# Kernel tuning notes

Hardware: AMD Instinct MI355X
Metric: run time of the kernel (lower is better)

The kernel has to match this reference:

```python
import jax, jax.numpy as jnp
import numpy as np

B, S, D, H = 2, 2048, 768, 12
E = D // H  # d_head = 64


def setup_inputs() -> dict:
    key = jax.random.key(0)
    ks = jax.random.split(key, 10)
    scale = 1.0 / np.sqrt(D)
    x = jax.random.normal(ks[0], (B, S, D), dtype=jnp.float32)
    # Additive mask, laid out [H*B, S, S] as the torch forward slices per head.
    attn_mask = jnp.zeros((H * B, S, S), dtype=jnp.float32)
    # Per-head projections (math form: q = x @ Wq[h] + bq[h])
    Wq = jax.random.normal(ks[1], (H, D, E), dtype=jnp.float32) * scale
    bq = jax.random.normal(ks[2], (H, E), dtype=jnp.float32) * 0.01
    Wk = jax.random.normal(ks[3], (H, D, E), dtype=jnp.float32) * scale
    bk = jax.random.normal(ks[4], (H, E), dtype=jnp.float32) * 0.01
    Wv = jax.random.normal(ks[5], (H, D, E), dtype=jnp.float32) * scale
    bv = jax.random.normal(ks[6], (H, E), dtype=jnp.float32) * 0.01
    Wo = jax.random.normal(ks[7], (D, D), dtype=jnp.float32) * scale
    bo = jax.random.normal(ks[8], (D,), dtype=jnp.float32) * 0.01
    return {"x": x, "attn_mask": attn_mask, "Wq": Wq, "bq": bq,
            "Wk": Wk, "bk": bk, "Wv": Wv, "bv": bv, "Wo": Wo, "bo": bo}


def reference(x, attn_mask, Wq, bq, Wk, bk, Wv, bv, Wo, bo):
    # x: [B,S,D]; attn_mask: [H*B,S,S]
    q = jnp.einsum('bsd,hde->hbse', x, Wq) + bq[:, None, None, :]
    k = jnp.einsum('bsd,hde->hbse', x, Wk) + bk[:, None, None, :]
    v = jnp.einsum('bsd,hde->hbse', x, Wv) + bv[:, None, None, :]
    mask = attn_mask.reshape(H, B, S, S)
    # NOTE: original code has NO 1/sqrt(d_head) scaling — kept faithful.
    logits = jnp.einsum('hbse,hbte->hbst', q, k) + mask
    w = jax.nn.softmax(logits, axis=-1)  # dropout is identity at eval / p=0
    o = jnp.einsum('hbst,hbte->hbse', w, v)  # [H,B,S,E]
    o = jnp.transpose(o, (1, 2, 0, 3)).reshape(B, S, H * E)  # concat heads
    return o @ Wo + bo
```

## Files before the change

kernel.cpp:

```cpp
#include <hip/hip_runtime.h>
#include <hip/hip_bf16.h>
#include <cmath>

constexpr int Bc  = 2;
constexpr int Sc  = 2048;
constexpr int Dc  = 768;
constexpr int Hc  = 12;
constexpr int Ec  = 64;
constexpr int BSc = Bc * Sc;

typedef _Float16 f16;
typedef __attribute__((ext_vector_type(8)))  _Float16 half8;
typedef __attribute__((ext_vector_type(16))) float    floatx16;

__global__ __launch_bounds__(256) void prep_kernel(
    const float* __restrict__ x,
    const float* __restrict__ Wq, const float* __restrict__ Wk, const float* __restrict__ Wv,
    const float* __restrict__ bq, const float* __restrict__ bk, const float* __restrict__ bv,
    const float* __restrict__ Wo,
    f16* __restrict__ x16, f16* __restrict__ Wt16, f16* __restrict__ Wot16,
    float* __restrict__ bias_cat)
{
    __shared__ __align__(16) float Ts[64][65];
    const int t = threadIdx.x;
    int bid = blockIdx.x;

    if (bid < 1536) {
        const size_t base = (size_t)bid * 2048 + t * 8;
        const float4 v0 = *(const float4*)(x + base);
        const float4 v1 = *(const float4*)(x + base + 4);
        half8 hv;
        hv[0] = (f16)v0.x; hv[1] = (f16)v0.y; hv[2] = (f16)v0.z; hv[3] = (f16)v0.w;
        hv[4] = (f16)v1.x; hv[5] = (f16)v1.y; hv[6] = (f16)v1.z; hv[7] = (f16)v1.w;
        *(half8*)(x16 + base) = hv;
        return;
    }
    bid -= 1536;
    if (bid < 432) {
        const int proj = bid / 144, rem = bid % 144, h = rem / 12, dt = rem % 12;
        const float* W = ((proj == 0) ? Wq : (proj == 1) ? Wk : Wv) + (size_t)h * Dc * Ec;
        const int c = t & 63, rr = t >> 6;
        #pragma unroll
        for (int r0 = 0; r0 < 64; r0 += 4) {
            const int d = rr + r0;
            Ts[d][c] = W[(size_t)(dt * 64 + d) * Ec + c];
        }
        __syncthreads();
        #pragma unroll
        for (int r0 = 0; r0 < 64; r0 += 4) {
            const int e = rr + r0;
            Wt16[(size_t)(proj * 768 + h * 64 + e) * Dc + dt * 64 + c] = (f16)Ts[c][e];
        }
        return;
    }
    bid -= 432;
    if (bid < 144) {
        const int rt = bid / 12, ct = bid % 12;
        const int c = t & 63, rr = t >> 6;
        #pragma unroll
        for (int r0 = 0; r0 < 64; r0 += 4) {
            const int d = rr + r0;
            Ts[d][c] = Wo[(size_t)(rt * 64 + d) * Dc + ct * 64 + c];
        }
        __syncthreads();
        #pragma unroll
        for (int r0 = 0; r0 < 64; r0 += 4) {
            const int e = rr + r0;
            Wot16[(size_t)(ct * 64 + e) * Dc + rt * 64 + c] = (f16)Ts[c][e];
        }
        return;
    }
    bid -= 144;
    {
        const int g = bid * 256 + t;
        if (g < 3 * 768) {
            const int proj = g / 768, idx = g % 768;
            const float* bb = (proj == 0) ? bq : (proj == 1) ? bk : bv;
            bias_cat[g] = bb[idx];
        }
    }
}

__global__ __launch_bounds__(256, 2) void gemm_qkv_kernel(
    const f16* __restrict__ x16, const f16* __restrict__ Wt16,
    const float* __restrict__ bias_cat,
    f16* __restrict__ q16, f16* __restrict__ k16, f16* __restrict__ v16t)
{
    __shared__ __align__(16) unsigned char smem[36864];
    f16 (*As)[72]  = (f16(*)[72])smem;
    f16 (*Bs)[72]  = (f16(*)[72])(smem + 18432);
    f16 (*Cs)[136] = (f16(*)[136])smem;

    const int t = threadIdx.x;
    const int wave = t >> 6, lane = t & 63;
    const int col = lane & 31, hf = lane >> 5;
    const int wr = wave & 1, wc = wave >> 1;
    const int m0 = blockIdx.x * 128, n0 = blockIdx.y * 128;

    floatx16 c00, c01, c10, c11;
    #pragma unroll
    for (int i = 0; i < 16; ++i) { c00[i] = 0.f; c01[i] = 0.f; c10[i] = 0.f; c11[i] = 0.f; }

    for (int k0 = 0; k0 < Dc; k0 += 64) {
        #pragma unroll
        for (int p = 0; p < 4; ++p) {
            const int cid = p * 256 + t;
            const int row = cid >> 3, seg = cid & 7;
            *(half8*)&As[row][seg * 8] =
                *(const half8*)(x16 + (size_t)(m0 + row) * Dc + k0 + seg * 8);
            *(half8*)&Bs[row][seg * 8] =
                *(const half8*)(Wt16 + (size_t)(n0 + row) * Dc + k0 + seg * 8);
        }
        __syncthreads();
        #pragma unroll
        for (int ks = 0; ks < 4; ++ks) {
            const half8 a0 = *(const half8*)&As[wr * 64 + col][ks * 16 + hf * 8];
            const half8 a1 = *(const half8*)&As[wr * 64 + 32 + col][ks * 16 + hf * 8];
            const half8 b0 = *(const half8*)&Bs[wc * 64 + col][ks * 16 + hf * 8];
            const half8 b1 = *(const half8*)&Bs[wc * 64 + 32 + col][ks * 16 + hf * 8];
            c00 = __builtin_amdgcn_mfma_f32_32x32x16_f16(a0, b0, c00, 0, 0, 0);
            c01 = __builtin_amdgcn_mfma_f32_32x32x16_f16(a0, b1, c01, 0, 0, 0);
            c10 = __builtin_amdgcn_mfma_f32_32x32x16_f16(a1, b0, c10, 0, 0, 0);
            c11 = __builtin_amdgcn_mfma_f32_32x32x16_f16(a1, b1, c11, 0, 0, 0);
        }
        __syncthreads();
    }

    const float bias0 = bias_cat[n0 + wc * 64 + col];
    const float bias1 = bias_cat[n0 + wc * 64 + 32 + col];
    #pragma unroll
    for (int i = 0; i < 16; ++i) {
        const int r = (i & 3) + 8 * (i >> 2) + 4 * hf;
        Cs[wr * 64 + r][wc * 64 + col]           = (f16)(c00[i] + bias0);
        Cs[wr * 64 + r][wc * 64 + 32 + col]      = (f16)(c01[i] + bias1);
        Cs[wr * 64 + 32 + r][wc * 64 + col]      = (f16)(c10[i] + bias0);
        Cs[wr * 64 + 32 + r][wc * 64 + 32 + col] = (f16)(c11[i] + bias1);
    }
    __syncthreads();

    const int proj = n0 / 768;
    const int h0   = (n0 - proj * 768) >> 6;
    const int b    = m0 >> 11;
    const int s_in = m0 & 2047;

    if (proj < 2) {
        f16* dst = (proj == 0) ? q16 : k16;
        const int row = t >> 1, seg = t & 1;
        const int h = h0 + seg;
        f16* gp = dst + ((size_t)(h * Bc + b) * Sc + s_in + row) * Ec;
        #pragma unroll
        for (int j = 0; j < 8; ++j)
            *(half8*)(gp + j * 8) = *(const half8*)&Cs[row][seg * 64 + j * 8];
    } else {
        const int coln = t & 127, half_ = t >> 7;
        const int seg = coln >> 6, e = coln & 63;
        const int h = h0 + seg;
        f16* gp = v16t + ((size_t)(h * Bc + b) * Ec + e) * Sc + s_in + half_ * 64;
        #pragma unroll
        for (int jb = 0; jb < 8; ++jb) {
            half8 tv;
            #pragma unroll
            for (int j2 = 0; j2 < 8; ++j2)
                tv[j2] = Cs[half_ * 64 + jb * 8 + j2][coln];
            *(half8*)(gp + jb * 8) = tv;
        }
    }
}

__global__ __launch_bounds__(256, 2) void flash_attn_kernel(
    const f16* __restrict__ q16, const f16* __restrict__ k16,
    const f16* __restrict__ v16t, const float* __restrict__ mask,
    f16* __restrict__ obuf16)
{
    __shared__ _Float16 Plds[4][32][40];
    __shared__ float MLds[2][64][17];
    __shared__ float LLds[2][64][17];
    __shared__ float OLds[2][64][33];

    const int rb   = blockIdx.x;
    const int b    = blockIdx.y;
    const int h    = blockIdx.z;
    const int hb   = h * Bc + b;
    const int t    = threadIdx.x;
    const int wave = t >> 6;
    const int lane = t & 63;
    const int rg   = wave & 1;
    const int kh   = wave >> 1;
    const int col  = lane & 31;
    const int hf   = lane >> 5;
    const int row0 = rb * 64 + rg * 32;

    const f16* qb = q16 + ((size_t)hb * Sc + row0) * Ec;
    const f16* kb = k16 + (size_t)hb * Sc * Ec;
    const f16* vb = v16t + (size_t)hb * Ec * Sc;

    half8 qfrag[4];
    #pragma unroll
    for (int ks = 0; ks < 4; ++ks)
        qfrag[ks] = *(const half8*)(qb + (size_t)col * Ec + ks * 16 + hf * 8);

    floatx16 o0, o1;
    float mrun[16], lrun[16];
    #pragma unroll
    for (int i = 0; i < 16; ++i) { o0[i] = 0.f; o1[i] = 0.f; mrun[i] = -1e30f; lrun[i] = 0.f; }

    const float* mbase = mask + ((size_t)hb * Sc + row0) * Sc + col;
    const int key_base = kh * (Sc / 2);
    constexpr int NT = (Sc / 2) / 32;

    float mbuf[16];
    #pragma unroll
    for (int i = 0; i < 16; ++i) {
        const int r = (i & 3) + 8 * (i >> 2) + 4 * hf;
        mbuf[i] = mbase[(size_t)r * Sc + key_base];
    }

    for (int kt = 0; kt < NT; ++kt) {
        const int key0 = key_base + kt * 32;

        float mcur[16];
        #pragma unroll
        for (int i = 0; i < 16; ++i) mcur[i] = mbuf[i];
        if (kt + 1 < NT) {
            #pragma unroll
            for (int i = 0; i < 16; ++i) {
                const int r = (i & 3) + 8 * (i >> 2) + 4 * hf;
                mbuf[i] = mbase[(size_t)r * Sc + key0 + 32];
            }
        }

        floatx16 c;
        #pragma unroll
        for (int i = 0; i < 16; ++i) c[i] = 0.f;
        #pragma unroll
        for (int ks = 0; ks < 4; ++ks) {
            const half8 kf = *(const half8*)(kb + (size_t)(key0 + col) * Ec + ks * 16 + hf * 8);
            c = __builtin_amdgcn_mfma_f32_32x32x16_f16(qfrag[ks], kf, c, 0, 0, 0);
        }

        float p[16];
        #pragma unroll
        for (int i = 0; i < 16; ++i) {
            const float s = c[i] + mcur[i];
            float v = s;
            v = fmaxf(v, __shfl_xor(v, 1));
            v = fmaxf(v, __shfl_xor(v, 2));
            v = fmaxf(v, __shfl_xor(v, 4));
            v = fmaxf(v, __shfl_xor(v, 8));
            v = fmaxf(v, __shfl_xor(v, 16));
            const float mnew  = fmaxf(mrun[i], v);
            const float alpha = __expf(mrun[i] - mnew);
            const float pe    = __expf(s - mnew);
            mrun[i] = mnew;
            float su = pe;
            su += __shfl_xor(su, 1);
            su += __shfl_xor(su, 2);
            su += __shfl_xor(su, 4);
            su += __shfl_xor(su, 8);
            su += __shfl_xor(su, 16);
            lrun[i] = lrun[i] * alpha + su;
            o0[i] *= alpha;
            o1[i] *= alpha;
            p[i] = pe;
        }

        #pragma unroll
        for (int i = 0; i < 16; ++i) {
            const int r = (i & 3) + 8 * (i >> 2) + 4 * hf;
            Plds[wave][r][col] = (f16)p[i];
        }
        asm volatile("s_waitcnt lgkmcnt(0)" ::: "memory");

        #pragma unroll
        for (int ks = 0; ks < 2; ++ks) {
            const half8 pf = *(const half8*)(&Plds[wave][col][ks * 16 + hf * 8]);
            const half8 v0 = *(const half8*)(vb + (size_t)col        * Sc + key0 + ks * 16 + hf * 8);
            const half8 v1 = *(const half8*)(vb + (size_t)(32 + col) * Sc + key0 + ks * 16 + hf * 8);
            o0 = __builtin_amdgcn_mfma_f32_32x32x16_f16(pf, v0, o0, 0, 0, 0);
            o1 = __builtin_amdgcn_mfma_f32_32x32x16_f16(pf, v1, o1, 0, 0, 0);
        }
    }

    if (kh == 1) {
        #pragma unroll
        for (int i = 0; i < 16; ++i) {
            MLds[rg][lane][i]      = mrun[i];
            LLds[rg][lane][i]      = lrun[i];
            OLds[rg][lane][i]      = o0[i];
            OLds[rg][lane][16 + i] = o1[i];
        }
    }
    __syncthreads();
    if (kh == 0) {
        #pragma unroll
        for (int i = 0; i < 16; ++i) {
            const float m2 = MLds[rg][lane][i];
            const float l2 = LLds[rg][lane][i];
            const float mn = fmaxf(mrun[i], m2);
            const float a1 = __expf(mrun[i] - mn);
            const float a2 = __expf(m2 - mn);
            const float inv = 1.f / (lrun[i] * a1 + l2 * a2);
            const float r0 = (o0[i] * a1 + OLds[rg][lane][i]      * a2) * inv;
            const float r1 = (o1[i] * a1 + OLds[rg][lane][16 + i] * a2) * inv;
            const int r = (i & 3) + 8 * (i >> 2) + 4 * hf;
            const size_t orow = ((size_t)b * Sc + row0 + r) * Dc + h * Ec;
            obuf16[orow + col]      = (f16)r0;
            obuf16[orow + 32 + col] = (f16)r1;
        }
    }
}

__global__ __launch_bounds__(256, 2) void gemm_out_kernel(
    const f16* __restrict__ a16, const f16* __restrict__ Wot16,
    const float* __restrict__ bo, float* __restrict__ out)
{
    __shared__ __align__(16) f16 As[128][72];
    __shared__ __align__(16) f16 Bs[64][72];

    const int t = threadIdx.x;
    const int wave = t >> 6, lane = t & 63;
    const int col = lane & 31, hf = lane >> 5;
    const int m0 = blockIdx.x * 128, n0 = blockIdx.y * 64;

    floatx16 c0, c1;
    #pragma unroll
    for (int i = 0; i < 16; ++i) { c0[i] = 0.f; c1[i] = 0.f; }

    for (int k0 = 0; k0 < Dc; k0 += 64) {
        #pragma unroll
        for (int p = 0; p < 4; ++p) {
            const int cid = p * 256 + t;
            *(half8*)&As[cid >> 3][(cid & 7) * 8] =
                *(const half8*)(a16 + (size_t)(m0 + (cid >> 3)) * Dc + k0 + (cid & 7) * 8);
        }
        #pragma unroll
        for (int p = 0; p < 2; ++p) {
            const int cid = p * 256 + t;
            *(half8*)&Bs[cid >> 3][(cid & 7) * 8] =
                *(const half8*)(Wot16 + (size_t)(n0 + (cid >> 3)) * Dc + k0 + (cid & 7) * 8);
        }
        __syncthreads();
        #pragma unroll
        for (int ks = 0; ks < 4; ++ks) {
            const half8 a  = *(const half8*)&As[wave * 32 + col][ks * 16 + hf * 8];
            const half8 b0 = *(const half8*)&Bs[col][ks * 16 + hf * 8];
            const half8 b1 = *(const half8*)&Bs[32 + col][ks * 16 + hf * 8];
            c0 = __builtin_amdgcn_mfma_f32_32x32x16_f16(a, b0, c0, 0, 0, 0);
            c1 = __builtin_amdgcn_mfma_f32_32x32x16_f16(a, b1, c1, 0, 0, 0);
        }
        __syncthreads();
    }

    const float bo0 = bo[n0 + col], bo1 = bo[n0 + 32 + col];
    #pragma unroll
    for (int i = 0; i < 16; ++i) {
        const int r = (i & 3) + 8 * (i >> 2) + 4 * hf;
        const size_t ro = (size_t)(m0 + wave * 32 + r) * Dc + n0;
        out[ro + col]      = c0[i] + bo0;
        out[ro + 32 + col] = c1[i] + bo1;
    }
}

extern "C" void kernel_launch(void* const* d_in, const int* in_sizes, int n_in,
                              void* d_out, int out_size, void* d_ws, size_t ws_size,
                              hipStream_t stream)
{
    const float* x    = (const float*)d_in[0];
    const float* mask = (const float*)d_in[1];
    const float* Wq   = (const float*)d_in[2];
    const float* bq   = (const float*)d_in[3];
    const float* Wk   = (const float*)d_in[4];
    const float* bk   = (const float*)d_in[5];
    const float* Wv   = (const float*)d_in[6];
    const float* bv   = (const float*)d_in[7];
    const float* Wo   = (const float*)d_in[8];
    const float* bo   = (const float*)d_in[9];
    float* out = (float*)d_out;

    constexpr size_t NQ = (size_t)Hc * Bc * Sc * Ec;
    f16* x16    = (f16*)d_ws;
    f16* Wt16   = x16 + (size_t)BSc * Dc;
    f16* Wot16  = Wt16 + (size_t)3 * Dc * Dc;
    f16* q16    = Wot16 + (size_t)Dc * Dc;
    f16* k16    = q16 + NQ;
    f16* v16t   = k16 + NQ;
    f16* obuf16 = v16t + NQ;
    float* bias_cat = (float*)(obuf16 + NQ);

    prep_kernel<<<2121, 256, 0, stream>>>(x, Wq, Wk, Wv, bq, bk, bv, Wo,
                                          x16, Wt16, Wot16, bias_cat);

    gemm_qkv_kernel<<<dim3(BSc / 128, 2304 / 128), 256, 0, stream>>>(
        x16, Wt16, bias_cat, q16, k16, v16t);

    flash_attn_kernel<<<dim3(Sc / 64, Bc, Hc), 256, 0, stream>>>(
        q16, k16, v16t, mask, obuf16);

    gemm_out_kernel<<<dim3(BSc / 128, Dc / 64), 256, 0, stream>>>(
        obuf16, Wot16, bo, out);
}
```

Baseline: 741.0 us.

## Use a two-pass softmax with a precomputed row max in flash attention

Adds a first pass over the keys that computes only QK^T to find each row's maximum, then shares it between the two key-half waves through LDS. The main loop then uses this fixed max, so it no longer needs per-tile max/sum shuffle reductions or rescaling of the output accumulators. Row sums are kept per lane and reduced once at the end, and the final merge becomes a plain add. In exchange the QK^T MFMAs and K loads are done twice. The max ignores the additive mask, which is safe for masks that are zero or negative but can overflow for large positive masks. The launch bound also asks for 3 blocks per CU instead of 2.

```diff
diff --git a/kernel.cpp b/kernel.cpp
--- a/kernel.cpp
+++ b/kernel.cpp
@@ -167,15 +167,15 @@
     }
 }
 
-__global__ __launch_bounds__(256, 2) void flash_attn_kernel(
+__global__ __launch_bounds__(256, 3) void flash_attn_kernel(
     const f16* __restrict__ q16, const f16* __restrict__ k16,
     const f16* __restrict__ v16t, const float* __restrict__ mask,
     f16* __restrict__ obuf16)
 {
     __shared__ _Float16 Plds[4][32][40];
-    __shared__ float MLds[2][64][17];
-    __shared__ float LLds[2][64][17];
-    __shared__ float OLds[2][64][33];
+    __shared__ float Msh[2][2][32];
+    __shared__ float Lsh[2][32];
+    __shared__ float OLsh[2][64][33];
 
     const int rb   = blockIdx.x;
     const int b    = blockIdx.y;
@@ -199,14 +199,57 @@
     for (int ks = 0; ks < 4; ++ks)
         qfrag[ks] = *(const half8*)(qb + (size_t)col * Ec + ks * 16 + hf * 8);
 
-    floatx16 o0, o1;
-    float mrun[16], lrun[16];
-    #pragma unroll
-    for (int i = 0; i < 16; ++i) { o0[i] = 0.f; o1[i] = 0.f; mrun[i] = -1e30f; lrun[i] = 0.f; }
-
-    const float* mbase = mask + ((size_t)hb * Sc + row0) * Sc + col;
     const int key_base = kh * (Sc / 2);
     constexpr int NT = (Sc / 2) / 32;
+
+    float vmax[16];
+    #pragma unroll
+    for (int i = 0; i < 16; ++i) vmax[i] = -3e38f;
+
+    for (int kt = 0; kt < NT; ++kt) {
+        const int key0 = key_base + kt * 32;
+        floatx16 c;
+        #pragma unroll
+        for (int i = 0; i < 16; ++i) c[i] = 0.f;
+        #pragma unroll
+        for (int ks = 0; ks < 4; ++ks) {
+            const half8 kf = *(const half8*)(kb + (size_t)(key0 + col) * Ec + ks * 16 + hf * 8);
+            c = __builtin_amdgcn_mfma_f32_32x32x16_f16(qfrag[ks], kf, c, 0, 0, 0);
+        }
+        #pragma unroll
+        for (int i = 0; i < 16; ++i) vmax[i] = fmaxf(vmax[i], c[i]);
+    }
+    #pragma unroll
+    for (int i = 0; i < 16; ++i) {
+        float v = vmax[i];
+        v = fmaxf(v, __shfl_xor(v, 1));
+        v = fmaxf(v, __shfl_xor(v, 2));
+        v = fmaxf(v, __shfl_xor(v, 4));
+        v = fmaxf(v, __shfl_xor(v, 8));
+        v = fmaxf(v, __shfl_xor(v, 16));
+        vmax[i] = v;
+    }
+    if (col == 0) {
+        #pragma unroll
+        for (int i = 0; i < 16; ++i) {
+            const int r = (i & 3) + 8 * (i >> 2) + 4 * hf;
+            Msh[kh][rg][r] = vmax[i];
+        }
+    }
+    __syncthreads();
+    float mrow[16];
+    #pragma unroll
+    for (int i = 0; i < 16; ++i) {
+        const int r = (i & 3) + 8 * (i >> 2) + 4 * hf;
+        mrow[i] = fmaxf(vmax[i], Msh[1 - kh][rg][r]);
+    }
+
+    floatx16 o0, o1;
+    float lsum[16];
+    #pragma unroll
+    for (int i = 0; i < 16; ++i) { o0[i] = 0.f; o1[i] = 0.f; lsum[i] = 0.f; }
+
+    const float* mbase = mask + ((size_t)hb * Sc + row0) * Sc + col;
 
     float mbuf[16];
     #pragma unroll
@@ -238,36 +281,12 @@
             c = __builtin_amdgcn_mfma_f32_32x32x16_f16(qfrag[ks], kf, c, 0, 0, 0);
         }
 
-        float p[16];
         #pragma unroll
         for (int i = 0; i < 16; ++i) {
-            const float s = c[i] + mcur[i];
-            float v = s;
-            v = fmaxf(v, __shfl_xor(v, 1));
-            v = fmaxf(v, __shfl_xor(v, 2));
-            v = fmaxf(v, __shfl_xor(v, 4));
-            v = fmaxf(v, __shfl_xor(v, 8));
-            v = fmaxf(v, __shfl_xor(v, 16));
-            const float mnew  = fmaxf(mrun[i], v);
-            const float alpha = __expf(mrun[i] - mnew);
-            const float pe    = __expf(s - mnew);
-            mrun[i] = mnew;
-            float su = pe;
-            su += __shfl_xor(su, 1);
-            su += __shfl_xor(su, 2);
-            su += __shfl_xor(su, 4);
-            su += __shfl_xor(su, 8);
-            su += __shfl_xor(su, 16);
-            lrun[i] = lrun[i] * alpha + su;
-            o0[i] *= alpha;
-            o1[i] *= alpha;
-            p[i] = pe;
-        }
-
-        #pragma unroll
-        for (int i = 0; i < 16; ++i) {
+            const float p = __expf(c[i] + mcur[i] - mrow[i]);
+            lsum[i] += p;
             const int r = (i & 3) + 8 * (i >> 2) + 4 * hf;
-            Plds[wave][r][col] = (f16)p[i];
+            Plds[wave][r][col] = (f16)p;
         }
         asm volatile("s_waitcnt lgkmcnt(0)" ::: "memory");
 
@@ -281,28 +300,39 @@
         }
     }
 
+    #pragma unroll
+    for (int i = 0; i < 16; ++i) {
+        float v = lsum[i];
+        v += __shfl_xor(v, 1);
+        v += __shfl_xor(v, 2);
+        v += __shfl_xor(v, 4);
+        v += __shfl_xor(v, 8);
+        v += __shfl_xor(v, 16);
+        lsum[i] = v;
+    }
+
     if (kh == 1) {
+        if (col == 0) {
+            #pragma unroll
+            for (int i = 0; i < 16; ++i) {
+                const int r = (i & 3) + 8 * (i >> 2) + 4 * hf;
+                Lsh[rg][r] = lsum[i];
+            }
+        }
         #pragma unroll
         for (int i = 0; i < 16; ++i) {
-            MLds[rg][lane][i]      = mrun[i];
-            LLds[rg][lane][i]      = lrun[i];
-            OLds[rg][lane][i]      = o0[i];
-            OLds[rg][lane][16 + i] = o1[i];
+            OLsh[rg][lane][i]      = o0[i];
+            OLsh[rg][lane][16 + i] = o1[i];
         }
     }
     __syncthreads();
     if (kh == 0) {
         #pragma unroll
         for (int i = 0; i < 16; ++i) {
-            const float m2 = MLds[rg][lane][i];
-            const float l2 = LLds[rg][lane][i];
-            const float mn = fmaxf(mrun[i], m2);
-            const float a1 = __expf(mrun[i] - mn);
-            const float a2 = __expf(m2 - mn);
-            const float inv = 1.f / (lrun[i] * a1 + l2 * a2);
-            const float r0 = (o0[i] * a1 + OLds[rg][lane][i]      * a2) * inv;
-            const float r1 = (o1[i] * a1 + OLds[rg][lane][16 + i] * a2) * inv;
             const int r = (i & 3) + 8 * (i >> 2) + 4 * hf;
+            const float inv = 1.f / (lsum[i] + Lsh[rg][r]);
+            const float r0 = (o0[i] + OLsh[rg][lane][i])      * inv;
+            const float r1 = (o1[i] + OLsh[rg][lane][16 + i]) * inv;
             const size_t orow = ((size_t)b * Sc + row0 + r) * Dc + h * Ec;
             obuf16[orow + col]      = (f16)r0;
             obuf16[orow + 32 + col] = (f16)r1;
```

Result: no change. 734.4 us (-0.9%).
